# Optimization experiments

Hardware: AMD Instinct MI355X
Metric: run time of the kernel (lower is better)

The kernel has to match this reference:

```python
import jax, jax.numpy as jnp
import numpy as np

EMBED_DIM = 1024
NUM_HEADS = 16
HEAD_DIM = EMBED_DIM // NUM_HEADS


def setup_inputs() -> dict:
    key = jax.random.key(0)
    ks = jax.random.split(key, 9)
    B, S, E = 2, 2048, EMBED_DIM
    scale = 1.0 / np.sqrt(E)
    x = jax.random.normal(ks[0], (B, S, E), dtype=jnp.float32)
    Wq = jax.random.normal(ks[1], (E, E), dtype=jnp.float32) * scale
    bq = jax.random.normal(ks[2], (E,), dtype=jnp.float32) * 0.01
    Wk = jax.random.normal(ks[3], (E, E), dtype=jnp.float32) * scale
    bk = jax.random.normal(ks[4], (E,), dtype=jnp.float32) * 0.01
    Wv = jax.random.normal(ks[5], (E, E), dtype=jnp.float32) * scale
    bv = jax.random.normal(ks[6], (E,), dtype=jnp.float32) * 0.01
    Wo = jax.random.normal(ks[7], (E, E), dtype=jnp.float32) * scale
    bo = jax.random.normal(ks[8], (E,), dtype=jnp.float32) * 0.01
    return {"x": x, "Wq": Wq, "bq": bq, "Wk": Wk, "bk": bk,
            "Wv": Wv, "bv": bv, "Wo": Wo, "bo": bo}


def reference(x, Wq, bq, Wk, bk, Wv, bv, Wo, bo):
    B, S, E = x.shape
    H, D = NUM_HEADS, HEAD_DIM
    # projections (torch Linear: x @ W.T + b), reshape to (B, H, S, D)
    q = (x @ Wq.T + bq).reshape(B, S, H, D).transpose(0, 2, 1, 3)
    k = (x @ Wk.T + bk).reshape(B, S, H, D).transpose(0, 2, 1, 3)
    v = (x @ Wv.T + bv).reshape(B, S, H, D).transpose(0, 2, 1, 3)
    softmax_scale = 1.0 / np.sqrt(D)
    # (B, H, S, S) scores, causal mask, stable softmax
    scores = softmax_scale * jnp.einsum('bhsd,bhtd->bhst', q, k)
    causal = jnp.tril(jnp.ones((S, S), dtype=bool))  # True = keep
    scores = jnp.where(causal, scores, -jnp.inf)
    attn = jax.nn.softmax(scores, axis=-1)
    out = jnp.einsum('bhst,bhtd->bhsd', attn, v)  # (B, H, S, D)
    out = out.transpose(0, 2, 1, 3).reshape(B, S, E)
    return out @ Wo.T + bo
```

## Files before the change

### kernel.cpp

```cpp
#include <hip/hip_runtime.h>
#include <cstdint>
#include <cstddef>

#define SEQ   2048
#define BATCH 2
#define EMB   1024
#define NH    16
#define HD    64
#define MTOT  (BATCH * SEQ)
#define NX    (MTOT * EMB)
#define NW    (EMB * EMB)
#define QS    3072

typedef __bf16 bf16_t;
typedef __bf16 bf16x2 __attribute__((ext_vector_type(2)));
typedef __bf16 bf16x4 __attribute__((ext_vector_type(4)));
typedef __bf16 bf16x8 __attribute__((ext_vector_type(8)));
typedef float  f32x4  __attribute__((ext_vector_type(4)));
typedef float  f32x16 __attribute__((ext_vector_type(16)));

typedef __attribute__((address_space(1))) const void* as1cv;
typedef __attribute__((address_space(3))) void*       as3v;

__device__ __forceinline__ void async_cp16(const void* g, void* l) {
  __builtin_amdgcn_global_load_lds((as1cv)g, (as3v)l, 16, 0, 0);
}

__device__ __forceinline__ f32x16 mfma32(bf16x8 a, bf16x8 b, f32x16 c) {
  return __builtin_amdgcn_mfma_f32_32x32x16_bf16(a, b, c, 0, 0, 0);
}

__device__ __forceinline__ uint32_t pk2(float a, float b) {
  bf16x2 t; t[0] = (bf16_t)a; t[1] = (bf16_t)b;
  return __builtin_bit_cast(uint32_t, t);
}
__device__ __forceinline__ bf16x8 mk_frag(uint32_t x, uint32_t y,
                                          uint32_t z, uint32_t w) {
  uint4 u; u.x = x; u.y = y; u.z = z; u.w = w;
  return __builtin_bit_cast(bf16x8, u);
}

__global__ __launch_bounds__(256) void cvt_all(
    const float* __restrict__ x,  const float* __restrict__ wq,
    const float* __restrict__ wk, const float* __restrict__ wv,
    const float* __restrict__ wo,
    bf16_t* __restrict__ xb,  bf16_t* __restrict__ wqb,
    bf16_t* __restrict__ wkb, bf16_t* __restrict__ wvb,
    bf16_t* __restrict__ wob) {
  long e = ((long)blockIdx.x * 256 + threadIdx.x) * 4;
  const float* s; bf16_t* d; long off;
  if (e < NX) { s = x; d = xb; off = e; }
  else {
    long e2 = e - NX;
    int w = (int)(e2 >> 20);
    off = e2 & (NW - 1);
    s = (w == 0) ? wq : (w == 1) ? wk : (w == 2) ? wv : wo;
    d = (w == 0) ? wqb : (w == 1) ? wkb : (w == 2) ? wvb : wob;
  }
  float4 v = *(const float4*)(s + off);
  bf16x4 o;
  o[0] = (bf16_t)v.x; o[1] = (bf16_t)v.y; o[2] = (bf16_t)v.z; o[3] = (bf16_t)v.w;
  *(bf16x4*)(d + off) = o;
}

__global__ __launch_bounds__(256) void vtrans(const bf16_t* __restrict__ QKV,
                                              bf16_t* __restrict__ VT) {
  const int hb = blockIdx.x;
  const int sb = blockIdx.y;
  const int h = hb & 15, b = hb >> 4;
  const int t = threadIdx.x;
  __shared__ __align__(16) bf16_t Ts[64 * 72];
  const bf16_t* Vp = QKV + ((size_t)(b * SEQ + sb * 64)) * QS + 2048 + h * HD;
  const int sr = t >> 4, d0 = (t & 15) * 4;
#pragma unroll
  for (int i = 0; i < 4; ++i) {
    bf16x4 v = *(const bf16x4*)(Vp + (size_t)(sr + 16 * i) * QS + d0);
    *(bf16x4*)&Ts[(sr + 16 * i) * 72 + d0] = v;
  }
  __syncthreads();
  const int d = t >> 2, tc = (t & 3) * 16;
  __align__(16) bf16_t out[16];
#pragma unroll
  for (int j = 0; j < 16; ++j) out[j] = Ts[(tc + j) * 72 + d];
  bf16_t* dst = VT + ((size_t)hb * HD + d) * SEQ + sb * 64 + tc;
  *(uint4*)(dst)     = *(uint4*)&out[0];
  *(uint4*)(dst + 8) = *(uint4*)&out[8];
}

template <typename OT, int BN, int CS>
__global__ __launch_bounds__(256) void gemm_f(
    const bf16_t* __restrict__ A, const bf16_t* __restrict__ Bw,
    const float* __restrict__ b0, const float* __restrict__ b1,
    const float* __restrict__ b2, OT* __restrict__ C) {
  constexpr int K = EMB, BK = 64;
  __shared__ __align__(16) bf16_t As[128 * BK];
  __shared__ __align__(16) bf16_t Bs[BN * BK];

  const int tid  = threadIdx.x;
  const int lane = tid & 63;
  const int wave = tid >> 6;
  const int l31  = lane & 31;
  const int hi   = lane >> 5;
  const int wm   = (wave >> 1) * 64;
  const int wn   = (wave & 1) * (BN / 2);
  const int m0   = blockIdx.y * 128;
  const int n0   = blockIdx.x * BN;

  const float* bias = (n0 < 1024) ? b0 : ((n0 < 2048) ? b1 : b2);

  const int row0 = tid >> 3, slot = tid & 7;
  const bf16_t* gA[4];
  const bf16_t* gB[BN / 32];
#pragma unroll
  for (int i = 0; i < 4; ++i)
    gA[i] = A + (size_t)(m0 + row0 + 32 * i) * K + (slot ^ (row0 & 7)) * 8;
#pragma unroll
  for (int i = 0; i < BN / 32; ++i)
    gB[i] = Bw + (size_t)(n0 + row0 + 32 * i) * K + (slot ^ (row0 & 7)) * 8;

  f32x16 acc[2][BN / 64] = {};
  const int sw = l31 & 7;

  for (int kk = 0; kk < K; kk += BK) {
#pragma unroll
    for (int i = 0; i < 4; ++i)
      async_cp16(gA[i] + kk, &As[(tid + 256 * i) * 8]);
#pragma unroll
    for (int i = 0; i < BN / 32; ++i)
      async_cp16(gB[i] + kk, &Bs[(tid + 256 * i) * 8]);
    __syncthreads();

#pragma unroll
    for (int ks = 0; ks < 4; ++ks) {
      const int js = ((ks * 2 + hi) ^ sw) * 8;
      bf16x8 af[2], bfr[BN / 64];
#pragma unroll
      for (int i = 0; i < 2; ++i)
        af[i] = *(const bf16x8*)&As[(wm + i * 32 + l31) * BK + js];
#pragma unroll
      for (int j = 0; j < BN / 64; ++j)
        bfr[j] = *(const bf16x8*)&Bs[(wn + j * 32 + l31) * BK + js];
#pragma unroll
      for (int i = 0; i < 2; ++i)
#pragma unroll
        for (int j = 0; j < BN / 64; ++j)
          acc[i][j] = mfma32(af[i], bfr[j], acc[i][j]);
    }
    __syncthreads();
  }

#pragma unroll
  for (int i = 0; i < 2; ++i)
#pragma unroll
    for (int j = 0; j < BN / 64; ++j) {
      const int col = n0 + wn + j * 32 + l31;
      const float bv = bias[col & 1023];
#pragma unroll
      for (int r = 0; r < 16; ++r) {
        const int row = m0 + wm + i * 32 + (r & 3) + 8 * (r >> 2) + 4 * hi;
        C[(size_t)row * CS + col] = (OT)(acc[i][j][r] + bv);
      }
    }
}

__global__ __launch_bounds__(256, 3) void attn128(
    const bf16_t* __restrict__ QKVg, const bf16_t* __restrict__ VTg,
    bf16_t* __restrict__ Og) {
  const int hb  = blockIdx.x;
  const int y   = blockIdx.y;
  const int s   = (y < 8) ? (15 - y) : (y - 8);
  const int h   = hb & 15, b = hb >> 4;
  const int tid = threadIdx.x;
  const int lane = tid & 63, wave = tid >> 6;
  const int l31 = lane & 31, hi = lane >> 5;
  const bool h0 = (hi == 0);

  __shared__ __align__(16) bf16_t Ks[2][64 * 72];
  __shared__ __align__(16) bf16_t VsT[2][64 * 72];
  __shared__ __align__(16) bf16_t Qs[128 * 64];

  const size_t base = ((size_t)b * SEQ) * QS + (size_t)h * HD;
  const bf16_t* Qb  = QKVg + base;
  const bf16_t* Kp  = QKVg + base + 1024;
  const bf16_t* VTp = VTg + (size_t)hb * HD * SEQ;

  const int kr0r = tid >> 3, kcol = (tid & 7) * 8;
  const int kr1r = kr0r + 32;
  const int lo0 = kr0r * 72 + kcol;
  const int lo1 = lo0 + 32 * 72;

  const int q0  = s * 128;
  const int nit = 2 * s + 2;
  const bf16_t* Qp = Qb + (size_t)q0 * QS;

  uint4 kr0 = *(const uint4*)(Kp + (size_t)kr0r * QS + kcol);
  uint4 kr1 = *(const uint4*)(Kp + (size_t)kr1r * QS + kcol);
  uint4 vr0 = *(const uint4*)(VTp + (size_t)kr0r * SEQ + kcol);
  uint4 vr1 = *(const uint4*)(VTp + (size_t)kr1r * SEQ + kcol);

#pragma unroll
  for (int i = 0; i < 4; ++i) {
    const int c = tid + 256 * i;
    *(uint4*)&Qs[(c >> 3) * 64 + (c & 7) * 8] =
        *(const uint4*)(Qp + (size_t)(c >> 3) * QS + (c & 7) * 8);
  }
  __syncthreads();

  bf16x8 qf[4];
#pragma unroll
  for (int kk = 0; kk < 4; ++kk)
    qf[kk] = *(const bf16x8*)&Qs[(32 * wave + l31) * 64 + kk * 16 + hi * 8];

  f32x16 acc_t0 = {}, acc_t1 = {};
  float lsum = 0.f;

  for (int it = 0; it < nit; ++it) {
    bf16_t* Kc = &Ks[it & 1][0];
    bf16_t* Vc = &VsT[it & 1][0];
    *(uint4*)&Kc[lo0] = kr0;
    *(uint4*)&Kc[lo1] = kr1;
    *(uint4*)&Vc[lo0] = vr0;
    *(uint4*)&Vc[lo1] = vr1;
    __syncthreads();

    if (it + 1 < nit) {
      const bf16_t* Kn  = Kp + (size_t)(it + 1) * 64 * QS;
      const bf16_t* VTn = VTp + (it + 1) * 64;
      kr0 = *(const uint4*)(Kn + (size_t)kr0r * QS + kcol);
      kr1 = *(const uint4*)(Kn + (size_t)kr1r * QS + kcol);
      vr0 = *(const uint4*)(VTn + (size_t)kr0r * SEQ + kcol);
      vr1 = *(const uint4*)(VTn + (size_t)kr1r * SEQ + kcol);
    }

    const bool active = (64 * it <= q0 + 32 * wave + 31);
    if (active) {
      f32x16 s0 = {}, s1 = {};
#pragma unroll
      for (int kk = 0; kk < 4; ++kk) {
        const bf16x8 kf0 = *(const bf16x8*)&Kc[l31 * 72 + kk * 16 + hi * 8];
        const bf16x8 kf1 =
            *(const bf16x8*)&Kc[(32 + l31) * 72 + kk * 16 + hi * 8];
        s0 = mfma32(kf0, qf[kk], s0);
        s1 = mfma32(kf1, qf[kk], s1);
      }

      constexpr float SC2 = 0.18033688011112042f;
      if (it >= nit - 2) {
        const int qg = q0 + 32 * wave + l31;
        const int k0 = 64 * it + 4 * hi;
#pragma unroll
        for (int r = 0; r < 16; ++r) {
          const int key = k0 + (r & 3) + 8 * (r >> 2);
          float p0 = exp2f(__builtin_fmaf(s0[r], SC2, -8.f));
          float p1 = exp2f(__builtin_fmaf(s1[r], SC2, -8.f));
          if (key > qg) p0 = 0.f;
          if (key + 32 > qg) p1 = 0.f;
          s0[r] = p0; s1[r] = p1;
          lsum += p0 + p1;
        }
      } else {
#pragma unroll
        for (int r = 0; r < 16; ++r) {
          const float p0 = exp2f(__builtin_fmaf(s0[r], SC2, -8.f));
          const float p1 = exp2f(__builtin_fmaf(s1[r], SC2, -8.f));
          s0[r] = p0; s1[r] = p1;
          lsum += p0 + p1;
        }
      }

      bf16x8 pf[4];
#pragma unroll
      for (int kk = 0; kk < 4; ++kk) {
        const f32x16& g = (kk < 2) ? s0 : s1;
        const int bir = 8 * (kk & 1);
        const uint32_t PL0 = pk2(g[bir + 0], g[bir + 1]);
        const uint32_t PL1 = pk2(g[bir + 2], g[bir + 3]);
        const uint32_t PH0 = pk2(g[bir + 4], g[bir + 5]);
        const uint32_t PH1 = pk2(g[bir + 6], g[bir + 7]);
        const uint32_t XL0 = (uint32_t)__shfl_xor((int)PL0, 32, 64);
        const uint32_t XL1 = (uint32_t)__shfl_xor((int)PL1, 32, 64);
        const uint32_t XH0 = (uint32_t)__shfl_xor((int)PH0, 32, 64);
        const uint32_t XH1 = (uint32_t)__shfl_xor((int)PH1, 32, 64);
        pf[kk] = h0 ? mk_frag(PL0, PL1, XL0, XL1)
                    : mk_frag(XH0, XH1, PH0, PH1);
      }

#pragma unroll
      for (int kk = 0; kk < 4; ++kk) {
        const bf16x8 vf0 = *(const bf16x8*)&Vc[l31 * 72 + kk * 16 + hi * 8];
        const bf16x8 vf1 =
            *(const bf16x8*)&Vc[(32 + l31) * 72 + kk * 16 + hi * 8];
        acc_t0 = mfma32(vf0, pf[kk], acc_t0);
        acc_t1 = mfma32(vf1, pf[kk], acc_t1);
      }
    }
  }

  const float lt = lsum + __shfl_xor(lsum, 32, 64);
  const float inv = 1.f / lt;
  bf16_t* Ow = &Qs[(32 * wave) * 64];
#pragma unroll
  for (int a = 0; a < 4; ++a)
#pragma unroll
    for (int c = 0; c < 4; c += 2) {
      const int r = 4 * a + c;
      const int d = c + 8 * a + 4 * hi;
      *(uint32_t*)&Ow[l31 * 64 + d] =
          pk2(acc_t0[r] * inv, acc_t0[r + 1] * inv);
      *(uint32_t*)&Ow[l31 * 64 + d + 32] =
          pk2(acc_t1[r] * inv, acc_t1[r + 1] * inv);
    }
  bf16_t* Op = Og + ((size_t)b * SEQ + q0 + 32 * wave) * EMB + (size_t)h * HD;
#pragma unroll
  for (int i = 0; i < 4; ++i) {
    const int id = lane + 64 * i;
    const int row = id >> 3, col8 = (id & 7) * 8;
    *(uint4*)(Op + (size_t)row * EMB + col8) =
        *(const uint4*)&Ow[row * 64 + col8];
  }
}

extern "C" void kernel_launch(void* const* d_in, const int* in_sizes, int n_in,
                              void* d_out, int out_size, void* d_ws,
                              size_t ws_size, hipStream_t stream) {
  const float* x  = (const float*)d_in[0];
  const float* Wq = (const float*)d_in[1];
  const float* bq = (const float*)d_in[2];
  const float* Wk = (const float*)d_in[3];
  const float* bk = (const float*)d_in[4];
  const float* Wv = (const float*)d_in[5];
  const float* bv = (const float*)d_in[6];
  const float* Wo = (const float*)d_in[7];
  const float* bo = (const float*)d_in[8];
  float* out = (float*)d_out;

  char* p = (char*)d_ws;
  bf16_t* xb   = (bf16_t*)p; p += (size_t)NX * 2;
  bf16_t* wqb  = (bf16_t*)p; p += (size_t)NW * 2;
  bf16_t* wkb  = (bf16_t*)p; p += (size_t)NW * 2;
  bf16_t* wvb  = (bf16_t*)p; p += (size_t)NW * 2;
  bf16_t* wob  = (bf16_t*)p; p += (size_t)NW * 2;
  bf16_t* qkvb = (bf16_t*)p; p += (size_t)NX * 3 * 2;
  bf16_t* ab   = (bf16_t*)p; p += (size_t)NX * 2;
  bf16_t* vtb  = xb;

  const int ntot = NX + 4 * NW;
  cvt_all<<<dim3(ntot / 4 / 256), 256, 0, stream>>>(
      x, Wq, Wk, Wv, Wo, xb, wqb, wkb, wvb, wob);

  gemm_f<bf16_t, 128, QS><<<dim3(QS / 128, MTOT / 128), 256, 0, stream>>>(
      xb, wqb, bq, bk, bv, qkvb);

  vtrans<<<dim3(BATCH * NH, SEQ / 64), 256, 0, stream>>>(qkvb, vtb);

  attn128<<<dim3(BATCH * NH, SEQ / 128), 256, 0, stream>>>(qkvb, vtb, ab);

  gemm_f<float, 64, EMB><<<dim3(EMB / 64, MTOT / 128), 256, 0, stream>>>(
      ab, wob, bo, bo, bo, out);
}
```

Before: 191.7 us.

## Split long causal attention rows across KV chunks with a combine pass

Query tiles with many KV iterations are split into up to four KV-range chunks that run as separate blocks from a static schedule table. Each chunk writes unnormalized fp32 partial outputs and row sums to a workspace, and a new combine kernel adds them and normalizes. The goal is to balance the triangular causal workload across 40 y-blocks instead of 16. Alongside this, the row sum is computed with an MFMA against a ones vector, the shuffle exchange is replaced with v_permlane32_swap, and setprio hints are added around the MFMAs. The cost is an extra kernel launch plus the write and reread of the fp32 partials.

After: 187.0 us. 2.5% less time.

```diff
diff --git a/kernel.cpp b/kernel.cpp
--- a/kernel.cpp
+++ b/kernel.cpp
@@ -11,6 +11,8 @@
 #define NX    (MTOT * EMB)
 #define NW    (EMB * EMB)
 #define QS    3072
+#define SLOTF 8448
+#define NSLOT 1152
 
 typedef __bf16 bf16_t;
 typedef __bf16 bf16x2 __attribute__((ext_vector_type(2)));
@@ -38,6 +40,10 @@
                                           uint32_t z, uint32_t w) {
   uint4 u; u.x = x; u.y = y; u.z = z; u.w = w;
   return __builtin_bit_cast(bf16x8, u);
+}
+
+__device__ __forceinline__ void plane_swap(uint32_t& a, uint32_t& b) {
+  asm("v_permlane32_swap_b32 %0, %1" : "+v"(a), "+v"(b));
 }
 
 __global__ __launch_bounds__(256) void cvt_all(
@@ -165,15 +171,32 @@
 
 __global__ __launch_bounds__(256, 3) void attn128(
     const bf16_t* __restrict__ QKVg, const bf16_t* __restrict__ VTg,
-    bf16_t* __restrict__ Og) {
+    bf16_t* __restrict__ Og, float* __restrict__ Pb) {
+  static const unsigned char St[40] = {
+      3, 7, 7, 10, 11, 11, 11, 14, 14, 15, 15, 15, 15,
+      6, 6, 9, 9, 10, 10, 12, 12, 13, 13, 13, 13, 14, 14,
+      2, 5, 5, 8, 8, 8, 9, 12, 12,
+      4, 4, 1, 0};
+  static const unsigned char Ct[40] = {
+      0, 0, 1, 0, 0, 1, 2, 0, 1, 0, 1, 2, 3,
+      0, 1, 0, 1, 1, 2, 0, 1, 0, 1, 2, 3, 2, 3,
+      0, 0, 1, 0, 1, 2, 2, 2, 3,
+      0, 1, 0, 0};
+  static const unsigned char cum[12] = {0, 2, 4, 6, 8, 11, 14, 17, 20, 24, 28, 32};
+
   const int hb  = blockIdx.x;
   const int y   = blockIdx.y;
-  const int s   = (y < 8) ? (15 - y) : (y - 8);
-  const int h   = hb & 15, b = hb >> 4;
+  const int s   = St[y], c = Ct[y];
+  const int nit = 2 * s + 2;
+  const int nch = (s >> 2) + 1;
+  const int bse = nit / nch;
+  const int rem = nit - bse * nch;
+  const int len = bse + (c < rem ? 1 : 0);
+  const int it0 = c * bse + (c < rem ? c : rem);
+  const int h = hb & 15, b = hb >> 4;
   const int tid = threadIdx.x;
   const int lane = tid & 63, wave = tid >> 6;
   const int l31 = lane & 31, hi = lane >> 5;
-  const bool h0 = (hi == 0);
 
   __shared__ __align__(16) bf16_t Ks[2][64 * 72];
   __shared__ __align__(16) bf16_t VsT[2][64 * 72];
@@ -190,19 +213,20 @@
   const int lo1 = lo0 + 32 * 72;
 
   const int q0  = s * 128;
-  const int nit = 2 * s + 2;
   const bf16_t* Qp = Qb + (size_t)q0 * QS;
 
-  uint4 kr0 = *(const uint4*)(Kp + (size_t)kr0r * QS + kcol);
-  uint4 kr1 = *(const uint4*)(Kp + (size_t)kr1r * QS + kcol);
-  uint4 vr0 = *(const uint4*)(VTp + (size_t)kr0r * SEQ + kcol);
-  uint4 vr1 = *(const uint4*)(VTp + (size_t)kr1r * SEQ + kcol);
+  const bf16_t* Kn0 = Kp + (size_t)it0 * 64 * QS;
+  const bf16_t* Vn0 = VTp + it0 * 64;
+  uint4 kr0 = *(const uint4*)(Kn0 + (size_t)kr0r * QS + kcol);
+  uint4 kr1 = *(const uint4*)(Kn0 + (size_t)kr1r * QS + kcol);
+  uint4 vr0 = *(const uint4*)(Vn0 + (size_t)kr0r * SEQ + kcol);
+  uint4 vr1 = *(const uint4*)(Vn0 + (size_t)kr1r * SEQ + kcol);
 
 #pragma unroll
   for (int i = 0; i < 4; ++i) {
-    const int c = tid + 256 * i;
-    *(uint4*)&Qs[(c >> 3) * 64 + (c & 7) * 8] =
-        *(const uint4*)(Qp + (size_t)(c >> 3) * QS + (c & 7) * 8);
+    const int cc = tid + 256 * i;
+    *(uint4*)&Qs[(cc >> 3) * 64 + (cc & 7) * 8] =
+        *(const uint4*)(Qp + (size_t)(cc >> 3) * QS + (cc & 7) * 8);
   }
   __syncthreads();
 
@@ -211,19 +235,24 @@
   for (int kk = 0; kk < 4; ++kk)
     qf[kk] = *(const bf16x8*)&Qs[(32 * wave + l31) * 64 + kk * 16 + hi * 8];
 
+  bf16x8 onef;
+#pragma unroll
+  for (int i = 0; i < 8; ++i) onef[i] = (bf16_t)1.0f;
+
   f32x16 acc_t0 = {}, acc_t1 = {};
-  float lsum = 0.f;
-
-  for (int it = 0; it < nit; ++it) {
-    bf16_t* Kc = &Ks[it & 1][0];
-    bf16_t* Vc = &VsT[it & 1][0];
+  f32x16 acc_l  = {};
+
+  for (int j = 0; j < len; ++j) {
+    const int it = it0 + j;
+    bf16_t* Kc = &Ks[j & 1][0];
+    bf16_t* Vc = &VsT[j & 1][0];
     *(uint4*)&Kc[lo0] = kr0;
     *(uint4*)&Kc[lo1] = kr1;
     *(uint4*)&Vc[lo0] = vr0;
     *(uint4*)&Vc[lo1] = vr1;
     __syncthreads();
 
-    if (it + 1 < nit) {
+    if (j + 1 < len) {
       const bf16_t* Kn  = Kp + (size_t)(it + 1) * 64 * QS;
       const bf16_t* VTn = VTp + (it + 1) * 64;
       kr0 = *(const uint4*)(Kn + (size_t)kr0r * QS + kcol);
@@ -235,6 +264,7 @@
     const bool active = (64 * it <= q0 + 32 * wave + 31);
     if (active) {
       f32x16 s0 = {}, s1 = {};
+      __builtin_amdgcn_s_setprio(1);
 #pragma unroll
       for (int kk = 0; kk < 4; ++kk) {
         const bf16x8 kf0 = *(const bf16x8*)&Kc[l31 * 72 + kk * 16 + hi * 8];
@@ -243,6 +273,7 @@
         s0 = mfma32(kf0, qf[kk], s0);
         s1 = mfma32(kf1, qf[kk], s1);
       }
+      __builtin_amdgcn_s_setprio(0);
 
       constexpr float SC2 = 0.18033688011112042f;
       if (it >= nit - 2) {
@@ -256,15 +287,12 @@
           if (key > qg) p0 = 0.f;
           if (key + 32 > qg) p1 = 0.f;
           s0[r] = p0; s1[r] = p1;
-          lsum += p0 + p1;
         }
       } else {
 #pragma unroll
         for (int r = 0; r < 16; ++r) {
-          const float p0 = exp2f(__builtin_fmaf(s0[r], SC2, -8.f));
-          const float p1 = exp2f(__builtin_fmaf(s1[r], SC2, -8.f));
-          s0[r] = p0; s1[r] = p1;
-          lsum += p0 + p1;
+          s0[r] = exp2f(__builtin_fmaf(s0[r], SC2, -8.f));
+          s1[r] = exp2f(__builtin_fmaf(s1[r], SC2, -8.f));
         }
       }
 
@@ -273,18 +301,16 @@
       for (int kk = 0; kk < 4; ++kk) {
         const f32x16& g = (kk < 2) ? s0 : s1;
         const int bir = 8 * (kk & 1);
-        const uint32_t PL0 = pk2(g[bir + 0], g[bir + 1]);
-        const uint32_t PL1 = pk2(g[bir + 2], g[bir + 3]);
-        const uint32_t PH0 = pk2(g[bir + 4], g[bir + 5]);
-        const uint32_t PH1 = pk2(g[bir + 6], g[bir + 7]);
-        const uint32_t XL0 = (uint32_t)__shfl_xor((int)PL0, 32, 64);
-        const uint32_t XL1 = (uint32_t)__shfl_xor((int)PL1, 32, 64);
-        const uint32_t XH0 = (uint32_t)__shfl_xor((int)PH0, 32, 64);
-        const uint32_t XH1 = (uint32_t)__shfl_xor((int)PH1, 32, 64);
-        pf[kk] = h0 ? mk_frag(PL0, PL1, XL0, XL1)
-                    : mk_frag(XH0, XH1, PH0, PH1);
-      }
-
+        uint32_t w0 = pk2(g[bir + 0], g[bir + 1]);
+        uint32_t w1 = pk2(g[bir + 2], g[bir + 3]);
+        uint32_t w2 = pk2(g[bir + 4], g[bir + 5]);
+        uint32_t w3 = pk2(g[bir + 6], g[bir + 7]);
+        plane_swap(w0, w2);
+        plane_swap(w1, w3);
+        pf[kk] = mk_frag(w0, w1, w2, w3);
+      }
+
+      __builtin_amdgcn_s_setprio(1);
 #pragma unroll
       for (int kk = 0; kk < 4; ++kk) {
         const bf16x8 vf0 = *(const bf16x8*)&Vc[l31 * 72 + kk * 16 + hi * 8];
@@ -292,31 +318,94 @@
             *(const bf16x8*)&Vc[(32 + l31) * 72 + kk * 16 + hi * 8];
         acc_t0 = mfma32(vf0, pf[kk], acc_t0);
         acc_t1 = mfma32(vf1, pf[kk], acc_t1);
-      }
-    }
-  }
-
-  const float lt = lsum + __shfl_xor(lsum, 32, 64);
-  const float inv = 1.f / lt;
-  bf16_t* Ow = &Qs[(32 * wave) * 64];
-#pragma unroll
-  for (int a = 0; a < 4; ++a)
-#pragma unroll
-    for (int c = 0; c < 4; c += 2) {
-      const int r = 4 * a + c;
-      const int d = c + 8 * a + 4 * hi;
-      *(uint32_t*)&Ow[l31 * 64 + d] =
-          pk2(acc_t0[r] * inv, acc_t0[r + 1] * inv);
-      *(uint32_t*)&Ow[l31 * 64 + d + 32] =
-          pk2(acc_t1[r] * inv, acc_t1[r + 1] * inv);
-    }
-  bf16_t* Op = Og + ((size_t)b * SEQ + q0 + 32 * wave) * EMB + (size_t)h * HD;
+        acc_l  = mfma32(onef, pf[kk], acc_l);
+      }
+      __builtin_amdgcn_s_setprio(0);
+    }
+  }
+
+  if (nch == 1) {
+    const float inv = 1.f / acc_l[0];
+    bf16_t* Ow = &Qs[(32 * wave) * 64];
+#pragma unroll
+    for (int aq = 0; aq < 4; ++aq)
+#pragma unroll
+      for (int cq = 0; cq < 4; cq += 2) {
+        const int r = 4 * aq + cq;
+        const int d = cq + 8 * aq + 4 * hi;
+        *(uint32_t*)&Ow[l31 * 64 + d] =
+            pk2(acc_t0[r] * inv, acc_t0[r + 1] * inv);
+        *(uint32_t*)&Ow[l31 * 64 + d + 32] =
+            pk2(acc_t1[r] * inv, acc_t1[r + 1] * inv);
+      }
+    bf16_t* Op = Og + ((size_t)b * SEQ + q0 + 32 * wave) * EMB + (size_t)h * HD;
+#pragma unroll
+    for (int i = 0; i < 4; ++i) {
+      const int id = lane + 64 * i;
+      const int row = id >> 3, col8 = (id & 7) * 8;
+      *(uint4*)(Op + (size_t)row * EMB + col8) =
+          *(const uint4*)&Ow[row * 64 + col8];
+    }
+  } else {
+    float* P = Pb + (size_t)(hb * 36 + cum[s - 4] + c) * SLOTF;
+#pragma unroll
+    for (int i = 0; i < 4; ++i) {
+      f32x4 v0, v1;
+#pragma unroll
+      for (int e = 0; e < 4; ++e) {
+        v0[e] = acc_t0[4 * i + e];
+        v1[e] = acc_t1[4 * i + e];
+      }
+      *(f32x4*)(P + (size_t)(i * 256 + tid) * 4)       = v0;
+      *(f32x4*)(P + (size_t)((4 + i) * 256 + tid) * 4) = v1;
+    }
+    P[8192 + tid] = acc_l[0];
+  }
+}
+
+__global__ __launch_bounds__(256) void attn_combine(
+    const float* __restrict__ Pb, bf16_t* __restrict__ Og) {
+  static const unsigned char cum[12] = {0, 2, 4, 6, 8, 11, 14, 17, 20, 24, 28, 32};
+  const int hb = blockIdx.x, sp = blockIdx.y;
+  const int s = sp + 4;
+  const int h = hb & 15, b = hb >> 4;
+  const int t = threadIdx.x;
+  const int lane = t & 63, wave = t >> 6;
+  const int l31 = lane & 31, hi = lane >> 5;
+  const int nch = (s >> 2) + 1;
+  const float* P0 = Pb + (size_t)(hb * 36 + cum[sp]) * SLOTF;
+
+  f32x4 a[8] = {};
+  float ls = 0.f;
+  for (int c = 0; c < nch; ++c) {
+    const float* P = P0 + (size_t)c * SLOTF;
+#pragma unroll
+    for (int i = 0; i < 8; ++i)
+      a[i] += *(const f32x4*)(P + (size_t)(i * 256 + t) * 4);
+    ls += P[8192 + t];
+  }
+  const float inv = 1.f / ls;
+
+  __shared__ __align__(16) bf16_t Ow[128 * 64];
+  bf16_t* Owp = &Ow[(32 * wave) * 64];
+#pragma unroll
+  for (int aq = 0; aq < 4; ++aq)
+#pragma unroll
+    for (int cq = 0; cq < 4; cq += 2) {
+      const int d = cq + 8 * aq + 4 * hi;
+      *(uint32_t*)&Owp[l31 * 64 + d] =
+          pk2(a[aq][cq] * inv, a[aq][cq + 1] * inv);
+      *(uint32_t*)&Owp[l31 * 64 + d + 32] =
+          pk2(a[4 + aq][cq] * inv, a[4 + aq][cq + 1] * inv);
+    }
+  bf16_t* Op =
+      Og + ((size_t)b * SEQ + 128 * s + 32 * wave) * EMB + (size_t)h * HD;
 #pragma unroll
   for (int i = 0; i < 4; ++i) {
     const int id = lane + 64 * i;
     const int row = id >> 3, col8 = (id & 7) * 8;
     *(uint4*)(Op + (size_t)row * EMB + col8) =
-        *(const uint4*)&Ow[row * 64 + col8];
+        *(const uint4*)&Owp[row * 64 + col8];
   }
 }
 
@@ -342,6 +431,7 @@
   bf16_t* wob  = (bf16_t*)p; p += (size_t)NW * 2;
   bf16_t* qkvb = (bf16_t*)p; p += (size_t)NX * 3 * 2;
   bf16_t* ab   = (bf16_t*)p; p += (size_t)NX * 2;
+  float*  pbuf = (float*)p;  p += (size_t)NSLOT * SLOTF * 4;
   bf16_t* vtb  = xb;
 
   const int ntot = NX + 4 * NW;
@@ -353,7 +443,9 @@
 
   vtrans<<<dim3(BATCH * NH, SEQ / 64), 256, 0, stream>>>(qkvb, vtb);
 
-  attn128<<<dim3(BATCH * NH, SEQ / 128), 256, 0, stream>>>(qkvb, vtb, ab);
+  attn128<<<dim3(BATCH * NH, 40), 256, 0, stream>>>(qkvb, vtb, ab, pbuf);
+
+  attn_combine<<<dim3(BATCH * NH, 12), 256, 0, stream>>>(pbuf, ab);
 
   gemm_f<float, 64, EMB><<<dim3(EMB / 64, MTOT / 128), 256, 0, stream>>>(
       ab, wob, bo, bo, bo, out);
```
